# Optimization experiments

Hardware: AMD Instinct MI355X
Metric: run time of the kernel (lower is better)

The kernel has to match this reference:

```python
import jax, jax.numpy as jnp
import numpy as np

D_K = 64

def setup_inputs() -> dict:
    key = jax.random.key(0)
    kq, kk, kv = jax.random.split(key, 3)
    B, Lq, Lk, d = 32, 2048, 2048, D_K
    return {
        "query": jax.random.normal(kq, (B, Lq, d), dtype=jnp.float32),
        "key": jax.random.normal(kk, (B, Lk, d), dtype=jnp.float32),
        "value": jax.random.normal(kv, (B, Lk, d), dtype=jnp.float32),
    }

def reference(query, key, value):
    d_k = query.shape[-1]
    scale = 1.0 / jnp.sqrt(jnp.asarray(d_k, query.dtype))
    scores = jnp.einsum('nqd,nkd->nqk', query, key) * scale  # (B, Lq, Lk)
    attn = jax.nn.softmax(scores, axis=-1)  # masked=None -> plain softmax; dropout p=0.0 is identity
    return jnp.einsum('nqk,nkd->nqd', attn, value)  # (B, Lq, d_v)
```

## Files before the change

kernel.cpp:

```cpp
#include <hip/hip_runtime.h>


#define NB   32
#define LSEQ 2048
#define DH   64
#define BM   64
#define BN   64
#define NIT  (LSEQ / BN)

typedef __attribute__((ext_vector_type(8)))  __bf16 bf16x8;
typedef __attribute__((ext_vector_type(16))) float  f32x16;
typedef __attribute__((ext_vector_type(2)))  unsigned uint2v;

union BF8 { bf16x8 v; unsigned short u[8]; unsigned u32[4]; uint4 q; };

__device__ __forceinline__ unsigned short f2bf(float f) {
    unsigned int u = __builtin_bit_cast(unsigned int, f);
    u += 0x7fffu + ((u >> 16) & 1u);
    return (unsigned short)(u >> 16);
}

__device__ __forceinline__ unsigned pack_bf2(float a, float b) {
    unsigned ua = __builtin_bit_cast(unsigned, a) + 0x8000u;
    unsigned ub = __builtin_bit_cast(unsigned, b) + 0x8000u;
    return __builtin_amdgcn_perm(ub, ua, 0x07060302u);
}

__device__ __forceinline__ float fast_exp2(float x) {
#if __has_builtin(__builtin_amdgcn_exp2f)
    return __builtin_amdgcn_exp2f(x);
#else
    return exp2f(x);
#endif
}

__device__ __forceinline__ void load_lds16(const void* g, void* l) {
    __builtin_amdgcn_global_load_lds(
        (const __attribute__((address_space(1))) void*)g,
        (__attribute__((address_space(3))) void*)l, 16, 0, 0);
}

#define KBLK ((NB * LSEQ * 8) / 256)
__global__ __launch_bounds__(256)
void prep(const float* __restrict__ Kg, const float* __restrict__ Vg,
          unsigned short* __restrict__ Kb, unsigned short* __restrict__ Vt) {
    __shared__ __align__(16) unsigned T2[64 * 36];
    const int tid = threadIdx.x;
    if (blockIdx.x < KBLK) {
        const int CH  = blockIdx.x * 256 + tid;
        const int b   = CH >> 14;
        const int rem = CH & 16383;
        const int n   = rem >> 3;
        const int cc  = rem & 7;
        const int c   = cc ^ (n & 7);
        const float* src = Kg + (((size_t)b * LSEQ + n) * DH + c * 8);
        float4 f0 = ((const float4*)src)[0];
        float4 f1 = ((const float4*)src)[1];
        BF8 t;
        t.u[0]=f2bf(f0.x); t.u[1]=f2bf(f0.y); t.u[2]=f2bf(f0.z); t.u[3]=f2bf(f0.w);
        t.u[4]=f2bf(f1.x); t.u[5]=f2bf(f1.y); t.u[6]=f2bf(f1.z); t.u[7]=f2bf(f1.w);
        *(bf16x8*)&Kb[(size_t)CH * 8] = t.v;
    } else {
        const int bx = blockIdx.x - KBLK;
        const int b  = bx >> 5;
        const int nt = bx & 31;
        const int n  = (tid >> 3) * 2;
        const int dc = (tid & 7) * 8;
        const float* s0 = Vg + (((size_t)b * LSEQ + nt * 64 + n) * DH + dc);
        float4 a0 = ((const float4*)s0)[0];
        float4 a1 = ((const float4*)s0)[1];
        const float* s1 = s0 + DH;
        float4 b0 = ((const float4*)s1)[0];
        float4 b1 = ((const float4*)s1)[1];
        float va[8] = {a0.x,a0.y,a0.z,a0.w, a1.x,a1.y,a1.z,a1.w};
        float vb[8] = {b0.x,b0.y,b0.z,b0.w, b1.x,b1.y,b1.z,b1.w};
        const int n2 = n >> 1;
        #pragma unroll
        for (int j = 0; j < 8; ++j)
            T2[(dc + j) * 36 + n2] = (unsigned)f2bf(va[j]) | ((unsigned)f2bf(vb[j]) << 16);
        __syncthreads();
        #pragma unroll
        for (int i = 0; i < 2; ++i) {
            const int CH = i * 256 + tid;
            const int cc = CH >> 6;
            const int d  = CH & 63;
            uint4 o = *(const uint4*)&T2[d * 36 + cc * 4];
            *(uint4*)&Vt[((((size_t)(b * 32 + nt)) * 8 + cc) * 64 + d) * 8] = o;
        }
    }
}

__global__ __launch_bounds__(256, 4)
void attn_fwd(const unsigned short* __restrict__ Kb,
              const unsigned short* __restrict__ Vt,
              const float* __restrict__ Qg,
              float* __restrict__ Og) {
    __shared__ __align__(16) char smem[18944];
    unsigned short* Kl = (unsigned short*)smem;
    float* Mrg = (float*)smem;
    float* Lsh = (float*)(smem + 18432);

    const int tid  = threadIdx.x;
    const int wave = tid >> 6;
    const int lane = tid & 63;
    const int m32  = lane & 31;
    const int h    = lane >> 5;
    const int qh   = wave >> 1;
    const int kvh  = wave & 1;

    const int L  = blockIdx.y * 32 + blockIdx.x;
    const int Lp = (L & 7) * 128 + (L >> 3);
    const int b  = Lp >> 5;
    const int qt = Lp & 31;

    const float qscale = 0.18033688011112042f;
    const int qrow = qt * BM + qh * 32 + m32;
    bf16x8 qf[4];
    {
        const float* qp = Qg + ((size_t)(b * LSEQ + qrow)) * DH;
        #pragma unroll
        for (int kt = 0; kt < 4; ++kt) {
            const float* p4 = qp + kt * 16 + h * 8;
            float4 f0 = ((const float4*)p4)[0];
            float4 f1 = ((const float4*)p4)[1];
            BF8 t;
            t.u[0]=f2bf(f0.x*qscale); t.u[1]=f2bf(f0.y*qscale);
            t.u[2]=f2bf(f0.z*qscale); t.u[3]=f2bf(f0.w*qscale);
            t.u[4]=f2bf(f1.x*qscale); t.u[5]=f2bf(f1.y*qscale);
            t.u[6]=f2bf(f1.z*qscale); t.u[7]=f2bf(f1.w*qscale);
            qf[kt] = t.v;
        }
    }

    int kidx[4];
    #pragma unroll
    for (int kt = 0; kt < 4; ++kt) {
        const int n  = kvh * 32 + m32;
        const int cc = kt * 2 + h;
        kidx[kt] = (n * 8 + (cc ^ (n & 7))) * 8;
    }

    const char* vgb = (const char*)Vt + (size_t)b * (32 * 8 * 64 * 16);
    const int v00 = (((kvh * 4 + 0 + h) * 64) +  0 + m32) * 16;
    const int v01 = (((kvh * 4 + 2 + h) * 64) +  0 + m32) * 16;
    const int v10 = (((kvh * 4 + 0 + h) * 64) + 32 + m32) * 16;
    const int v11 = (((kvh * 4 + 2 + h) * 64) + 32 + m32) * 16;

    const char* kgb = (const char*)Kb + (size_t)b * (LSEQ * DH * 2);
    const int CH0 = wave * 128 + lane;
    const int CH1 = CH0 + 64;

    {
        char* kd = smem + wave * 2048;
        load_lds16(kgb + CH0 * 16, kd);
        load_lds16(kgb + CH1 * 16, kd + 1024);
    }

    f32x16 o0, o1;
    #pragma unroll
    for (int i = 0; i < 16; ++i) { o0[i] = 0.f; o1[i] = 0.f; }
    float l_run = 0.f;

    for (int nt = 0; nt < NIT; ++nt) {
        const int cur = nt & 1;
        __syncthreads();

        BF8 vf00, vf01, vf10, vf11;
        {
            const char* vp = vgb + nt * 8192;
            vf00.q = *(const uint4*)(vp + v00);
            vf01.q = *(const uint4*)(vp + v01);
            vf10.q = *(const uint4*)(vp + v10);
            vf11.q = *(const uint4*)(vp + v11);
        }

        if (nt + 1 < NIT) {
            char* kd = smem + (cur ^ 1) * 8192 + wave * 2048;
            load_lds16(kgb + (nt + 1) * 8192 + CH0 * 16, kd);
            load_lds16(kgb + (nt + 1) * 8192 + CH1 * 16, kd + 1024);
        }

        const unsigned short* kb = Kl + cur * 4096;
        f32x16 s;
        #pragma unroll
        for (int i = 0; i < 16; ++i) s[i] = 0.f;
        __builtin_amdgcn_s_setprio(1);
        #pragma unroll
        for (int kt = 0; kt < 4; ++kt) {
            bf16x8 kf = *(const bf16x8*)&kb[kidx[kt]];
            s = __builtin_amdgcn_mfma_f32_32x32x16_bf16(kf, qf[kt], s, 0, 0, 0);
        }
        __builtin_amdgcn_s_setprio(0);

        unsigned pk[8];
        #pragma unroll
        for (int g = 0; g < 4; ++g) {
            float e0 = fast_exp2(s[4*g]);
            float e1 = fast_exp2(s[4*g+1]);
            float e2 = fast_exp2(s[4*g+2]);
            float e3 = fast_exp2(s[4*g+3]);
            l_run += ((e0 + e1) + (e2 + e3));
            pk[2*g]   = pack_bf2(e0, e1);
            pk[2*g+1] = pack_bf2(e2, e3);
        }

        BF8 p0, p1;
#if __has_builtin(__builtin_amdgcn_permlane32_swap)
        {
            uint2v r;
            r = __builtin_amdgcn_permlane32_swap(pk[0], pk[2], false, false);
            p0.u32[0] = r[0]; p0.u32[2] = r[1];
            r = __builtin_amdgcn_permlane32_swap(pk[1], pk[3], false, false);
            p0.u32[1] = r[0]; p0.u32[3] = r[1];
            r = __builtin_amdgcn_permlane32_swap(pk[4], pk[6], false, false);
            p1.u32[0] = r[0]; p1.u32[2] = r[1];
            r = __builtin_amdgcn_permlane32_swap(pk[5], pk[7], false, false);
            p1.u32[1] = r[0]; p1.u32[3] = r[1];
        }
#else
        {
            const unsigned sA0 = h ? pk[0] : pk[2];
            const unsigned sA1 = h ? pk[1] : pk[3];
            const unsigned sB0 = h ? pk[4] : pk[6];
            const unsigned sB1 = h ? pk[5] : pk[7];
            const unsigned rA0 = __shfl_xor((int)sA0, 32, 64);
            const unsigned rA1 = __shfl_xor((int)sA1, 32, 64);
            const unsigned rB0 = __shfl_xor((int)sB0, 32, 64);
            const unsigned rB1 = __shfl_xor((int)sB1, 32, 64);
            p0.u32[0] = h ? rA0 : pk[0];  p0.u32[1] = h ? rA1 : pk[1];
            p0.u32[2] = h ? pk[2] : rA0;  p0.u32[3] = h ? pk[3] : rA1;
            p1.u32[0] = h ? rB0 : pk[4];  p1.u32[1] = h ? rB1 : pk[5];
            p1.u32[2] = h ? pk[6] : rB0;  p1.u32[3] = h ? pk[7] : rB1;
        }
#endif

        __builtin_amdgcn_s_setprio(1);
        o0 = __builtin_amdgcn_mfma_f32_32x32x16_bf16(vf00.v, p0.v, o0, 0, 0, 0);
        o0 = __builtin_amdgcn_mfma_f32_32x32x16_bf16(vf01.v, p1.v, o0, 0, 0, 0);
        o1 = __builtin_amdgcn_mfma_f32_32x32x16_bf16(vf10.v, p0.v, o1, 0, 0, 0);
        o1 = __builtin_amdgcn_mfma_f32_32x32x16_bf16(vf11.v, p1.v, o1, 0, 0, 0);
        __builtin_amdgcn_s_setprio(0);
    }

    const float l2 = l_run + __shfl_xor(l_run, 32, 64);
    __syncthreads();
    if (kvh) {
        float* mp = Mrg + ((size_t)qh * 64 + lane) * 36;
        #pragma unroll
        for (int g = 0; g < 4; ++g) {
            *(float4*)(mp + 4*g)      = (float4){o0[4*g], o0[4*g+1], o0[4*g+2], o0[4*g+3]};
            *(float4*)(mp + 16 + 4*g) = (float4){o1[4*g], o1[4*g+1], o1[4*g+2], o1[4*g+3]};
        }
        if (h == 0) Lsh[qh * 32 + m32] = l2;
    }
    __syncthreads();
    if (!kvh) {
        const float* mp = Mrg + ((size_t)qh * 64 + lane) * 36;
        #pragma unroll
        for (int g = 0; g < 4; ++g) {
            float4 a = *(const float4*)(mp + 4*g);
            float4 c = *(const float4*)(mp + 16 + 4*g);
            o0[4*g] += a.x; o0[4*g+1] += a.y; o0[4*g+2] += a.z; o0[4*g+3] += a.w;
            o1[4*g] += c.x; o1[4*g+1] += c.y; o1[4*g+2] += c.z; o1[4*g+3] += c.w;
        }
        const float inv = 1.0f / (l2 + Lsh[qh * 32 + m32]);
        float* op = Og + ((size_t)(b * LSEQ + qrow)) * DH;
        #pragma unroll
        for (int t = 0; t < 2; ++t)
            #pragma unroll
            for (int g = 0; g < 4; ++g) {
                float4 v;
                v.x = (t ? o1[4*g+0] : o0[4*g+0]) * inv;
                v.y = (t ? o1[4*g+1] : o0[4*g+1]) * inv;
                v.z = (t ? o1[4*g+2] : o0[4*g+2]) * inv;
                v.w = (t ? o1[4*g+3] : o0[4*g+3]) * inv;
                *(float4*)(op + t * 32 + g * 8 + h * 4) = v;
            }
    }
}

extern "C" void kernel_launch(void* const* d_in, const int* in_sizes, int n_in,
                              void* d_out, int out_size, void* d_ws, size_t ws_size,
                              hipStream_t stream) {
    const float* Q = (const float*)d_in[0];
    const float* K = (const float*)d_in[1];
    const float* V = (const float*)d_in[2];
    float* O = (float*)d_out;

    unsigned short* Kb = (unsigned short*)d_ws;
    unsigned short* Vt = (unsigned short*)d_ws + 4u * 1024u * 1024u;

    prep<<<dim3(KBLK + NB * (LSEQ / 64)), dim3(256), 0, stream>>>(K, V, Kb, Vt);
    attn_fwd<<<dim3(LSEQ / BM, NB), dim3(256), 0, stream>>>(Kb, Vt, Q, O);
}
```

Before: 137.2 us.

## Give each wave private K LDS buffers, prefetch V a tile ahead, drop per-tile barriers

Each wave now loads its own copy of the K rows it needs into a private double-buffered LDS region, which removes the block-wide __syncthreads in the KV loop and replaces it with explicit vmcnt waits. V fragments are prefetched one tile ahead into alternating register sets through a 2x manually unrolled loop. The bf16 packing now uses the compiler's native conversion instead of a bias-and-permute trick, and the first QK MFMA starts from a zero accumulator. In exchange, LDS use grows to 32 KB per block, K is loaded redundantly across the two query-half waves, more registers are held live, and correctness depends on the hand-placed vmcnt counts.

```diff
diff --git a/kernel.cpp b/kernel.cpp
--- a/kernel.cpp
+++ b/kernel.cpp
@@ -20,10 +20,10 @@
     return (unsigned short)(u >> 16);
 }
 
-__device__ __forceinline__ unsigned pack_bf2(float a, float b) {
-    unsigned ua = __builtin_bit_cast(unsigned, a) + 0x8000u;
-    unsigned ub = __builtin_bit_cast(unsigned, b) + 0x8000u;
-    return __builtin_amdgcn_perm(ub, ua, 0x07060302u);
+__device__ __forceinline__ unsigned cvt_pk_bf16(float a, float b) {
+    union { __bf16 h[2]; unsigned u; } t;
+    t.h[0] = (__bf16)a; t.h[1] = (__bf16)b;
+    return t.u;
 }
 
 __device__ __forceinline__ float fast_exp2(float x) {
@@ -95,7 +95,7 @@
               const unsigned short* __restrict__ Vt,
               const float* __restrict__ Qg,
               float* __restrict__ Og) {
-    __shared__ __align__(16) char smem[18944];
+    __shared__ __align__(16) char smem[32768];
     unsigned short* Kl = (unsigned short*)smem;
     float* Mrg = (float*)smem;
     float* Lsh = (float*)(smem + 18432);
@@ -135,9 +135,8 @@
     int kidx[4];
     #pragma unroll
     for (int kt = 0; kt < 4; ++kt) {
-        const int n  = kvh * 32 + m32;
         const int cc = kt * 2 + h;
-        kidx[kt] = (n * 8 + (cc ^ (n & 7))) * 8;
+        kidx[kt] = (m32 * 8 + (cc ^ (m32 & 7))) * 8;
     }
 
     const char* vgb = (const char*)Vt + (size_t)b * (32 * 8 * 64 * 16);
@@ -147,100 +146,90 @@
     const int v11 = (((kvh * 4 + 2 + h) * 64) + 32 + m32) * 16;
 
     const char* kgb = (const char*)Kb + (size_t)b * (LSEQ * DH * 2);
-    const int CH0 = wave * 128 + lane;
-    const int CH1 = CH0 + 64;
-
+    char* const kbase = smem + wave * 8192;
+
+    BF8 vfa[4], vfb[4];
     {
-        char* kd = smem + wave * 2048;
-        load_lds16(kgb + CH0 * 16, kd);
-        load_lds16(kgb + CH1 * 16, kd + 1024);
-    }
-
-    f32x16 o0, o1;
+        const char* ks = kgb + kvh * 4096 + lane * 16;
+        load_lds16(ks,        kbase);
+        load_lds16(ks + 1024, kbase + 1024);
+        load_lds16(ks + 2048, kbase + 2048);
+        load_lds16(ks + 3072, kbase + 3072);
+        vfa[0].q = *(const uint4*)(vgb + v00);
+        vfa[1].q = *(const uint4*)(vgb + v01);
+        vfa[2].q = *(const uint4*)(vgb + v10);
+        vfa[3].q = *(const uint4*)(vgb + v11);
+    }
+
+    f32x16 o0, o1, fz;
     #pragma unroll
-    for (int i = 0; i < 16; ++i) { o0[i] = 0.f; o1[i] = 0.f; }
+    for (int i = 0; i < 16; ++i) { o0[i] = 0.f; o1[i] = 0.f; fz[i] = 0.f; }
     float l_run = 0.f;
 
-    for (int nt = 0; nt < NIT; ++nt) {
-        const int cur = nt & 1;
-        __syncthreads();
-
-        BF8 vf00, vf01, vf10, vf11;
-        {
-            const char* vp = vgb + nt * 8192;
-            vf00.q = *(const uint4*)(vp + v00);
-            vf01.q = *(const uint4*)(vp + v01);
-            vf10.q = *(const uint4*)(vp + v10);
-            vf11.q = *(const uint4*)(vp + v11);
-        }
-
-        if (nt + 1 < NIT) {
-            char* kd = smem + (cur ^ 1) * 8192 + wave * 2048;
-            load_lds16(kgb + (nt + 1) * 8192 + CH0 * 16, kd);
-            load_lds16(kgb + (nt + 1) * 8192 + CH1 * 16, kd + 1024);
-        }
-
-        const unsigned short* kb = Kl + cur * 4096;
-        f32x16 s;
-        #pragma unroll
-        for (int i = 0; i < 16; ++i) s[i] = 0.f;
-        __builtin_amdgcn_s_setprio(1);
-        #pragma unroll
-        for (int kt = 0; kt < 4; ++kt) {
-            bf16x8 kf = *(const bf16x8*)&kb[kidx[kt]];
-            s = __builtin_amdgcn_mfma_f32_32x32x16_bf16(kf, qf[kt], s, 0, 0, 0);
-        }
-        __builtin_amdgcn_s_setprio(0);
-
-        unsigned pk[8];
-        #pragma unroll
-        for (int g = 0; g < 4; ++g) {
-            float e0 = fast_exp2(s[4*g]);
-            float e1 = fast_exp2(s[4*g+1]);
-            float e2 = fast_exp2(s[4*g+2]);
-            float e3 = fast_exp2(s[4*g+3]);
-            l_run += ((e0 + e1) + (e2 + e3));
-            pk[2*g]   = pack_bf2(e0, e1);
-            pk[2*g+1] = pack_bf2(e2, e3);
-        }
-
-        BF8 p0, p1;
-#if __has_builtin(__builtin_amdgcn_permlane32_swap)
-        {
-            uint2v r;
-            r = __builtin_amdgcn_permlane32_swap(pk[0], pk[2], false, false);
-            p0.u32[0] = r[0]; p0.u32[2] = r[1];
-            r = __builtin_amdgcn_permlane32_swap(pk[1], pk[3], false, false);
-            p0.u32[1] = r[0]; p0.u32[3] = r[1];
-            r = __builtin_amdgcn_permlane32_swap(pk[4], pk[6], false, false);
-            p1.u32[0] = r[0]; p1.u32[2] = r[1];
-            r = __builtin_amdgcn_permlane32_swap(pk[5], pk[7], false, false);
-            p1.u32[1] = r[0]; p1.u32[3] = r[1];
-        }
-#else
-        {
-            const unsigned sA0 = h ? pk[0] : pk[2];
-            const unsigned sA1 = h ? pk[1] : pk[3];
-            const unsigned sB0 = h ? pk[4] : pk[6];
-            const unsigned sB1 = h ? pk[5] : pk[7];
-            const unsigned rA0 = __shfl_xor((int)sA0, 32, 64);
-            const unsigned rA1 = __shfl_xor((int)sA1, 32, 64);
-            const unsigned rB0 = __shfl_xor((int)sB0, 32, 64);
-            const unsigned rB1 = __shfl_xor((int)sB1, 32, 64);
-            p0.u32[0] = h ? rA0 : pk[0];  p0.u32[1] = h ? rA1 : pk[1];
-            p0.u32[2] = h ? pk[2] : rA0;  p0.u32[3] = h ? pk[3] : rA1;
-            p1.u32[0] = h ? rB0 : pk[4];  p1.u32[1] = h ? rB1 : pk[5];
-            p1.u32[2] = h ? pk[6] : rB0;  p1.u32[3] = h ? pk[7] : rB1;
-        }
-#endif
-
-        __builtin_amdgcn_s_setprio(1);
-        o0 = __builtin_amdgcn_mfma_f32_32x32x16_bf16(vf00.v, p0.v, o0, 0, 0, 0);
-        o0 = __builtin_amdgcn_mfma_f32_32x32x16_bf16(vf01.v, p1.v, o0, 0, 0, 0);
-        o1 = __builtin_amdgcn_mfma_f32_32x32x16_bf16(vf10.v, p0.v, o1, 0, 0, 0);
-        o1 = __builtin_amdgcn_mfma_f32_32x32x16_bf16(vf11.v, p1.v, o1, 0, 0, 0);
-        __builtin_amdgcn_s_setprio(0);
-    }
+#define BODY(NT_, CUR_, VFC, VFN)                                              \
+    {                                                                          \
+        if ((NT_) + 1 < NIT) {     \
+            char* kd = kbase + ((CUR_) ^ 1) * 4096;                            \
+            const char* ks = kgb + ((NT_) + 1) * 8192 + kvh * 4096 + lane * 16;\
+            load_lds16(ks,        kd);                                         \
+            load_lds16(ks + 1024, kd + 1024);                                  \
+            load_lds16(ks + 2048, kd + 2048);                                  \
+            load_lds16(ks + 3072, kd + 3072);                                  \
+            const char* vp = vgb + ((NT_) + 1) * 8192;                         \
+            VFN[0].q = *(const uint4*)(vp + v00);                              \
+            VFN[1].q = *(const uint4*)(vp + v01);                              \
+            VFN[2].q = *(const uint4*)(vp + v10);                              \
+            VFN[3].q = *(const uint4*)(vp + v11);                              \
+                  \
+            asm volatile("s_waitcnt vmcnt(8)" ::: "memory");                   \
+        } else {                                                               \
+            asm volatile("s_waitcnt vmcnt(0)" ::: "memory");                   \
+        }                                                                      \
+        const unsigned short* kb = Kl + wave * 4096 + (CUR_) * 2048;           \
+        __builtin_amdgcn_s_setprio(1);                                         \
+        bf16x8 kf0 = *(const bf16x8*)&kb[kidx[0]];                             \
+        f32x16 s = __builtin_amdgcn_mfma_f32_32x32x16_bf16(kf0, qf[0], fz, 0, 0, 0); \
+        _Pragma("unroll")                                                      \
+        for (int kt = 1; kt < 4; ++kt) {                                       \
+            bf16x8 kf = *(const bf16x8*)&kb[kidx[kt]];                         \
+            s = __builtin_amdgcn_mfma_f32_32x32x16_bf16(kf, qf[kt], s, 0, 0, 0); \
+        }                                                                      \
+        __builtin_amdgcn_s_setprio(0);                                         \
+        float e[16];                                                           \
+        _Pragma("unroll")                                                      \
+        for (int r = 0; r < 16; ++r) e[r] = fast_exp2(s[r]);                   \
+        unsigned pk[8];                                                        \
+        _Pragma("unroll")                                                      \
+        for (int g = 0; g < 4; ++g) {                                          \
+            l_run += ((e[4*g] + e[4*g+1]) + (e[4*g+2] + e[4*g+3]));            \
+            pk[2*g]   = cvt_pk_bf16(e[4*g],   e[4*g+1]);                       \
+            pk[2*g+1] = cvt_pk_bf16(e[4*g+2], e[4*g+3]);                       \
+        }                                                                      \
+        BF8 p0, p1;                                                            \
+        {                                                                      \
+            uint2v r;                                                          \
+            r = __builtin_amdgcn_permlane32_swap(pk[0], pk[2], false, false);  \
+            p0.u32[0] = r[0]; p0.u32[2] = r[1];                                \
+            r = __builtin_amdgcn_permlane32_swap(pk[1], pk[3], false, false);  \
+            p0.u32[1] = r[0]; p0.u32[3] = r[1];                                \
+            r = __builtin_amdgcn_permlane32_swap(pk[4], pk[6], false, false);  \
+            p1.u32[0] = r[0]; p1.u32[2] = r[1];                                \
+            r = __builtin_amdgcn_permlane32_swap(pk[5], pk[7], false, false);  \
+            p1.u32[1] = r[0]; p1.u32[3] = r[1];                                \
+        }                                                                      \
+        __builtin_amdgcn_s_setprio(1);                                         \
+        o0 = __builtin_amdgcn_mfma_f32_32x32x16_bf16(VFC[0].v, p0.v, o0, 0, 0, 0); \
+        o0 = __builtin_amdgcn_mfma_f32_32x32x16_bf16(VFC[1].v, p1.v, o0, 0, 0, 0); \
+        o1 = __builtin_amdgcn_mfma_f32_32x32x16_bf16(VFC[2].v, p0.v, o1, 0, 0, 0); \
+        o1 = __builtin_amdgcn_mfma_f32_32x32x16_bf16(VFC[3].v, p1.v, o1, 0, 0, 0); \
+        __builtin_amdgcn_s_setprio(0);                                         \
+    }
+
+    for (int nt = 0; nt < NIT; nt += 2) {
+        BODY(nt,     0, vfa, vfb);
+        BODY(nt + 1, 1, vfb, vfa);
+    }
+#undef BODY
 
     const float l2 = l_run + __shfl_xor(l_run, 32, 64);
     __syncthreads();
```

New measurement: 144.2 us. 1.05x slower.

## Load K fragments directly from global into registers, drop LDS staging and barriers

Applied to the files above, without the earlier changes.

Removes the LDS double-buffer for K tiles and the per-iteration __syncthreads. Each wave now loads its K and V fragments straight from global memory into registers, prefetching the next tile right after the MFMAs that consume the current one. It also switches P packing to native bf16 conversion and uses nontemporal loads for Q and nontemporal stores for O. Dropping the barrier gives waves freedom to run independently, but it raises register pressure and makes both waves of a KV half fetch the same K rows from global memory (through cache) rather than sharing one LDS copy.

```diff
diff --git a/kernel.cpp b/kernel.cpp
--- a/kernel.cpp
+++ b/kernel.cpp
@@ -10,6 +10,7 @@
 
 typedef __attribute__((ext_vector_type(8)))  __bf16 bf16x8;
 typedef __attribute__((ext_vector_type(16))) float  f32x16;
+typedef __attribute__((ext_vector_type(4)))  float  f32x4;
 typedef __attribute__((ext_vector_type(2)))  unsigned uint2v;
 
 union BF8 { bf16x8 v; unsigned short u[8]; unsigned u32[4]; uint4 q; };
@@ -20,10 +21,10 @@
     return (unsigned short)(u >> 16);
 }
 
-__device__ __forceinline__ unsigned pack_bf2(float a, float b) {
-    unsigned ua = __builtin_bit_cast(unsigned, a) + 0x8000u;
-    unsigned ub = __builtin_bit_cast(unsigned, b) + 0x8000u;
-    return __builtin_amdgcn_perm(ub, ua, 0x07060302u);
+__device__ __forceinline__ unsigned cvt_pk_bf16(float a, float b) {
+    union { __bf16 h[2]; unsigned u; } t;
+    t.h[0] = (__bf16)a; t.h[1] = (__bf16)b;
+    return t.u;
 }
 
 __device__ __forceinline__ float fast_exp2(float x) {
@@ -32,12 +33,6 @@
 #else
     return exp2f(x);
 #endif
-}
-
-__device__ __forceinline__ void load_lds16(const void* g, void* l) {
-    __builtin_amdgcn_global_load_lds(
-        (const __attribute__((address_space(1))) void*)g,
-        (__attribute__((address_space(3))) void*)l, 16, 0, 0);
 }
 
 #define KBLK ((NB * LSEQ * 8) / 256)
@@ -96,13 +91,12 @@
               const float* __restrict__ Qg,
               float* __restrict__ Og) {
     __shared__ __align__(16) char smem[18944];
-    unsigned short* Kl = (unsigned short*)smem;
     float* Mrg = (float*)smem;
     float* Lsh = (float*)(smem + 18432);
 
     const int tid  = threadIdx.x;
+    const int lane = tid & 63;
     const int wave = tid >> 6;
-    const int lane = tid & 63;
     const int m32  = lane & 31;
     const int h    = lane >> 5;
     const int qh   = wave >> 1;
@@ -121,8 +115,8 @@
         #pragma unroll
         for (int kt = 0; kt < 4; ++kt) {
             const float* p4 = qp + kt * 16 + h * 8;
-            float4 f0 = ((const float4*)p4)[0];
-            float4 f1 = ((const float4*)p4)[1];
+            f32x4 f0 = __builtin_nontemporal_load((const f32x4*)p4);
+            f32x4 f1 = __builtin_nontemporal_load(((const f32x4*)p4) + 1);
             BF8 t;
             t.u[0]=f2bf(f0.x*qscale); t.u[1]=f2bf(f0.y*qscale);
             t.u[2]=f2bf(f0.z*qscale); t.u[3]=f2bf(f0.w*qscale);
@@ -132,29 +126,29 @@
         }
     }
 
-    int kidx[4];
+    int koff[4];
     #pragma unroll
     for (int kt = 0; kt < 4; ++kt) {
         const int n  = kvh * 32 + m32;
         const int cc = kt * 2 + h;
-        kidx[kt] = (n * 8 + (cc ^ (n & 7))) * 8;
-    }
-
-    const char* vgb = (const char*)Vt + (size_t)b * (32 * 8 * 64 * 16);
+        koff[kt] = (n * 8 + (cc ^ (n & 7))) * 16;
+    }
+
     const int v00 = (((kvh * 4 + 0 + h) * 64) +  0 + m32) * 16;
     const int v01 = (((kvh * 4 + 2 + h) * 64) +  0 + m32) * 16;
     const int v10 = (((kvh * 4 + 0 + h) * 64) + 32 + m32) * 16;
     const int v11 = (((kvh * 4 + 2 + h) * 64) + 32 + m32) * 16;
 
     const char* kgb = (const char*)Kb + (size_t)b * (LSEQ * DH * 2);
-    const int CH0 = wave * 128 + lane;
-    const int CH1 = CH0 + 64;
-
-    {
-        char* kd = smem + wave * 2048;
-        load_lds16(kgb + CH0 * 16, kd);
-        load_lds16(kgb + CH1 * 16, kd + 1024);
-    }
+    const char* vgb = (const char*)Vt + (size_t)b * (DH * LSEQ * 2);
+
+    BF8 kf[4], vf[4];
+    #pragma unroll
+    for (int kt = 0; kt < 4; ++kt) kf[kt].q = *(const uint4*)(kgb + koff[kt]);
+    vf[0].q = *(const uint4*)(vgb + v00);
+    vf[1].q = *(const uint4*)(vgb + v01);
+    vf[2].q = *(const uint4*)(vgb + v10);
+    vf[3].q = *(const uint4*)(vgb + v11);
 
     f32x16 o0, o1;
     #pragma unroll
@@ -162,35 +156,20 @@
     float l_run = 0.f;
 
     for (int nt = 0; nt < NIT; ++nt) {
-        const int cur = nt & 1;
-        __syncthreads();
-
-        BF8 vf00, vf01, vf10, vf11;
-        {
-            const char* vp = vgb + nt * 8192;
-            vf00.q = *(const uint4*)(vp + v00);
-            vf01.q = *(const uint4*)(vp + v01);
-            vf10.q = *(const uint4*)(vp + v10);
-            vf11.q = *(const uint4*)(vp + v11);
-        }
-
-        if (nt + 1 < NIT) {
-            char* kd = smem + (cur ^ 1) * 8192 + wave * 2048;
-            load_lds16(kgb + (nt + 1) * 8192 + CH0 * 16, kd);
-            load_lds16(kgb + (nt + 1) * 8192 + CH1 * 16, kd + 1024);
-        }
-
-        const unsigned short* kb = Kl + cur * 4096;
         f32x16 s;
         #pragma unroll
         for (int i = 0; i < 16; ++i) s[i] = 0.f;
         __builtin_amdgcn_s_setprio(1);
         #pragma unroll
-        for (int kt = 0; kt < 4; ++kt) {
-            bf16x8 kf = *(const bf16x8*)&kb[kidx[kt]];
-            s = __builtin_amdgcn_mfma_f32_32x32x16_bf16(kf, qf[kt], s, 0, 0, 0);
-        }
+        for (int kt = 0; kt < 4; ++kt)
+            s = __builtin_amdgcn_mfma_f32_32x32x16_bf16(kf[kt].v, qf[kt], s, 0, 0, 0);
         __builtin_amdgcn_s_setprio(0);
+
+        if (nt + 1 < NIT) {
+            const char* kp = kgb + (nt + 1) * 8192;
+            #pragma unroll
+            for (int kt = 0; kt < 4; ++kt) kf[kt].q = *(const uint4*)(kp + koff[kt]);
+        }
 
         unsigned pk[8];
         #pragma unroll
@@ -200,12 +179,11 @@
             float e2 = fast_exp2(s[4*g+2]);
             float e3 = fast_exp2(s[4*g+3]);
             l_run += ((e0 + e1) + (e2 + e3));
-            pk[2*g]   = pack_bf2(e0, e1);
-            pk[2*g+1] = pack_bf2(e2, e3);
+            pk[2*g]   = cvt_pk_bf16(e0, e1);
+            pk[2*g+1] = cvt_pk_bf16(e2, e3);
         }
 
         BF8 p0, p1;
-#if __has_builtin(__builtin_amdgcn_permlane32_swap)
         {
             uint2v r;
             r = __builtin_amdgcn_permlane32_swap(pk[0], pk[2], false, false);
@@ -217,29 +195,21 @@
             r = __builtin_amdgcn_permlane32_swap(pk[5], pk[7], false, false);
             p1.u32[1] = r[0]; p1.u32[3] = r[1];
         }
-#else
-        {
-            const unsigned sA0 = h ? pk[0] : pk[2];
-            const unsigned sA1 = h ? pk[1] : pk[3];
-            const unsigned sB0 = h ? pk[4] : pk[6];
-            const unsigned sB1 = h ? pk[5] : pk[7];
-            const unsigned rA0 = __shfl_xor((int)sA0, 32, 64);
-            const unsigned rA1 = __shfl_xor((int)sA1, 32, 64);
-            const unsigned rB0 = __shfl_xor((int)sB0, 32, 64);
-            const unsigned rB1 = __shfl_xor((int)sB1, 32, 64);
-            p0.u32[0] = h ? rA0 : pk[0];  p0.u32[1] = h ? rA1 : pk[1];
-            p0.u32[2] = h ? pk[2] : rA0;  p0.u32[3] = h ? pk[3] : rA1;
-            p1.u32[0] = h ? rB0 : pk[4];  p1.u32[1] = h ? rB1 : pk[5];
-            p1.u32[2] = h ? pk[6] : rB0;  p1.u32[3] = h ? pk[7] : rB1;
-        }
-#endif
 
         __builtin_amdgcn_s_setprio(1);
-        o0 = __builtin_amdgcn_mfma_f32_32x32x16_bf16(vf00.v, p0.v, o0, 0, 0, 0);
-        o0 = __builtin_amdgcn_mfma_f32_32x32x16_bf16(vf01.v, p1.v, o0, 0, 0, 0);
-        o1 = __builtin_amdgcn_mfma_f32_32x32x16_bf16(vf10.v, p0.v, o1, 0, 0, 0);
-        o1 = __builtin_amdgcn_mfma_f32_32x32x16_bf16(vf11.v, p1.v, o1, 0, 0, 0);
+        o0 = __builtin_amdgcn_mfma_f32_32x32x16_bf16(vf[0].v, p0.v, o0, 0, 0, 0);
+        o0 = __builtin_amdgcn_mfma_f32_32x32x16_bf16(vf[1].v, p1.v, o0, 0, 0, 0);
+        o1 = __builtin_amdgcn_mfma_f32_32x32x16_bf16(vf[2].v, p0.v, o1, 0, 0, 0);
+        o1 = __builtin_amdgcn_mfma_f32_32x32x16_bf16(vf[3].v, p1.v, o1, 0, 0, 0);
         __builtin_amdgcn_s_setprio(0);
+
+        if (nt + 1 < NIT) {
+            const char* vp = vgb + (nt + 1) * 8192;
+            vf[0].q = *(const uint4*)(vp + v00);
+            vf[1].q = *(const uint4*)(vp + v01);
+            vf[2].q = *(const uint4*)(vp + v10);
+            vf[3].q = *(const uint4*)(vp + v11);
+        }
     }
 
     const float l2 = l_run + __shfl_xor(l_run, 32, 64);
@@ -269,12 +239,12 @@
         for (int t = 0; t < 2; ++t)
             #pragma unroll
             for (int g = 0; g < 4; ++g) {
-                float4 v;
+                f32x4 v;
                 v.x = (t ? o1[4*g+0] : o0[4*g+0]) * inv;
                 v.y = (t ? o1[4*g+1] : o0[4*g+1]) * inv;
                 v.z = (t ? o1[4*g+2] : o0[4*g+2]) * inv;
                 v.w = (t ? o1[4*g+3] : o0[4*g+3]) * inv;
-                *(float4*)(op + t * 32 + g * 8 + h * 4) = v;
+                __builtin_nontemporal_store(v, (f32x4*)(op + t * 32 + g * 8 + h * 4));
             }
     }
 }
```

Result: slower. 142.6 us (+3.9%).
